# Performance work log

Hardware: AMD Instinct MI355X
Metric: run time of the kernel (lower is better)

The kernel has to match this reference:

```python
import jax, jax.numpy as jnp
import numpy as np

N, CIN, COUT = 8, 256, 512
HEADS, DK, DV = 8, 256, 256
MAP = 32          # H = W = map_size
KS, PAD = 3, 1
DKH = DK // HEADS  # 32
DVH = DV // HEADS  # 32
CONV_OUT = COUT - DV  # 256


def conv2d(x, w, b, stride=1, padding=0):
    out = jax.lax.conv_general_dilated(
        x, w, (stride, stride), [(padding, padding), (padding, padding)],
        dimension_numbers=("NCHW", "OIHW", "NCHW"))
    return out + b[None, :, None, None]


def rel_to_abs(x):
    # x: [B, G, L, 2L-1] relative logits -> [B, G, L, L] absolute (skewing trick)
    B, G, L, _ = x.shape
    x = jnp.pad(x, ((0, 0), (0, 0), (0, 0), (0, 1)))          # [B,G,L,2L]
    flat = x.reshape(B, G, L * 2 * L)
    flat = jnp.pad(flat, ((0, 0), (0, 0), (0, L - 1)))
    return flat.reshape(B, G, L + 1, 2 * L - 1)[:, :, :L, L - 1:]


def setup_inputs() -> dict:
    key = jax.random.key(0)
    ks = jax.random.split(key, 16)
    def w(k, shape, fan_in):
        return jax.random.normal(k, shape, jnp.float32) * (fan_in ** -0.5)
    inp = {
        "x": jax.random.normal(ks[0], (N, CIN, MAP, MAP), jnp.float32),
        "conv_w": w(ks[1], (CONV_OUT, CIN, KS, KS), CIN * KS * KS),
        "conv_b": jnp.zeros((CONV_OUT,), jnp.float32),
        "q_w": w(ks[2], (DK, CIN, KS, KS), CIN * KS * KS),
        "q_b": jnp.zeros((DK,), jnp.float32),
        "k_w": w(ks[3], (DK, CIN, KS, KS), CIN * KS * KS),
        "k_b": jnp.zeros((DK,), jnp.float32),
        "v_w": w(ks[4], (DV, CIN, KS, KS), CIN * KS * KS),
        "v_b": jnp.zeros((DV,), jnp.float32),
        "attn_w": w(ks[5], (DV, DV, 1, 1), DV),
        "attn_b": jnp.zeros((DV,), jnp.float32),
        "width_mat": jax.random.normal(ks[6], (2 * MAP - 1, DKH), jnp.float32) * (DKH ** -0.5),
        "height_mat": jax.random.normal(ks[7], (2 * MAP - 1, DKH), jnp.float32) * (DKH ** -0.5),
    }
    return inp


def reference(x, conv_w, conv_b, q_w, q_b, k_w, k_b, v_w, v_b,
              attn_w, attn_b, width_mat, height_mat):
    conv_maps = conv2d(x, conv_w, conv_b, 1, PAD)            # [N, 256, H, W]
    H = W = MAP
    q = conv2d(x, q_w, q_b, 1, PAD).reshape(N, HEADS, DKH, H, W)
    k = conv2d(x, k_w, k_b, 1, PAD).reshape(N, HEADS, DKH, H, W)
    v = conv2d(x, v_w, v_b, 1, PAD).reshape(N, HEADS, DVH, H, W)

    qf = q.reshape(N, HEADS, DKH, H * W)
    kf = k.reshape(N, HEADS, DKH, H * W)
    vf = v.reshape(N, HEADS, DVH, H * W)
    logits = jnp.einsum("nhdq,nhdk->nhqk", qf, kf)           # [N,h,HW,HW]

    qp = q.transpose(0, 1, 3, 4, 2)                          # [N,h,H,W,dkh]
    # width relative logits: depends on (hq, wq, wk), broadcast over hk
    rel_w = jnp.einsum("nhyxd,rd->nhyxr", qp, width_mat)     # [N,h,H,W,2W-1]
    abs_w = rel_to_abs(rel_w.reshape(N, HEADS * H, W, 2 * W - 1)
                       ).reshape(N, HEADS, H, W, W)          # [N,h,hq,wq,wk]
    # height relative logits: depends on (wq, hq, hk), broadcast over wk
    rel_h = jnp.einsum("nhyxd,rd->nhxyr", qp, height_mat)    # [N,h,W,H,2H-1]
    abs_h = rel_to_abs(rel_h.reshape(N, HEADS * W, H, 2 * H - 1)
                       ).reshape(N, HEADS, W, H, H)          # [N,h,wq,hq,hk]

    w_bias = abs_w[:, :, :, :, None, :]                      # [N,h,hq,wq,1,wk]
    h_bias = abs_h.transpose(0, 1, 3, 2, 4)[..., None]       # [N,h,hq,wq,hk,1]
    logits = (logits.reshape(N, HEADS, H, W, H, W) + h_bias + w_bias
              ).reshape(N, HEADS, H * W, H * W)
    logits = logits * (DKH ** -0.5)

    weights = jax.nn.softmax(logits, axis=-1)
    attn = jnp.einsum("nhqk,nhdk->nhqd", weights, vf)        # [N,h,HW,dvh]
    # faithful to torch .view quirk: row-major reshape [HW,dvh] -> [dvh,H,W]
    attn_maps = attn.reshape(N, HEADS * DVH, H, W)
    attn_maps = conv2d(attn_maps, attn_w, attn_b, 1, 0)
    return jnp.concatenate([conv_maps, attn_maps], axis=1)
```

## Files before the change

kernel.cpp:

```cpp
#include <hip/hip_runtime.h>
#include <hip/hip_bf16.h>


typedef __attribute__((ext_vector_type(8))) __bf16 bf16x8;
typedef __attribute__((ext_vector_type(4))) float f32x4;
typedef unsigned short u16;
typedef unsigned int u32;
typedef __attribute__((ext_vector_type(8))) u16 u16x8;

#define GLD(gp, lp) __builtin_amdgcn_global_load_lds( \
    (const __attribute__((address_space(1))) u32*)(gp), \
    (__attribute__((address_space(3))) u32*)(lp), 16, 0, 0)

static __device__ __forceinline__ u16 f2bf(float f) {
  u32 u = __builtin_bit_cast(u32, f);
  u += 0x7fffu + ((u >> 16) & 1u);
  return (u16)(u >> 16);
}
static __device__ __forceinline__ float bf2f(u16 h) {
  return __builtin_bit_cast(float, (u32)h << 16);
}

__global__ void k_cast_w(const float* __restrict__ conv_w, const float* __restrict__ q_w,
                         const float* __restrict__ k_w, const float* __restrict__ v_w,
                         const float* __restrict__ attn_w,
                         u16* __restrict__ W9, u16* __restrict__ W1) {
  int stride = gridDim.x * blockDim.x;
  for (int t = blockIdx.x * blockDim.x + threadIdx.x; t < 1024 * 2304; t += stride) {
    int row = t / 2304;
    int rem = t - row * 2304;
    int t9 = rem >> 8, c = rem & 255;
    const float* src = row < 256 ? conv_w : row < 512 ? q_w : row < 768 ? k_w : v_w;
    W9[t] = f2bf(src[(row & 255) * 2304 + c * 9 + t9]);
  }
  for (int t = blockIdx.x * blockDim.x + threadIdx.x; t < 256 * 256; t += stride)
    W1[t] = f2bf(attn_w[t]);
}

__global__ void k_xT(const float* __restrict__ x, u16* __restrict__ xT,
                     u16* __restrict__ zpage) {
  if (blockIdx.x == 0 && threadIdx.x < 512) zpage[threadIdx.x] = 0;
  __shared__ float t[32][33];
  int b = blockIdx.x;
  int sb = b & 31, cb = (b >> 5) & 7, n = b >> 8;
  int s0 = sb << 5, c0 = cb << 5;
  int ls = threadIdx.x & 31, lc = threadIdx.x >> 5;
#pragma unroll
  for (int i = 0; i < 4; ++i) {
    int c = lc + i * 8;
    t[c][ls] = x[(((n << 8) + c0 + c) << 10) + s0 + ls];
  }
  __syncthreads();
#pragma unroll
  for (int i = 0; i < 4; ++i) {
    int s = lc + i * 8;
    xT[(((n << 10) + s0 + s) << 8) + c0 + ls] = f2bf(t[ls][s]);
  }
}

__global__ __launch_bounds__(256) void k_gemm_conv(
    const u16* __restrict__ A, const u16* __restrict__ xT, const u16* __restrict__ zpage,
    float* __restrict__ out,
    u16* __restrict__ qb, u16* __restrict__ kb, u16* __restrict__ vb,
    const float* __restrict__ conv_b, const float* __restrict__ q_b,
    const float* __restrict__ k_b, const float* __restrict__ v_b) {
  __shared__ u16 As[8192], Bs[8192];
  f32x4 acc[4][4] = {};
  const int tid = threadIdx.x;
  const int wave = tid >> 6, lane = tid & 63;
  const int wr = wave >> 1, wc = wave & 1;
  const int lr = lane & 15, lk = lane >> 4;
  const int srow = lane >> 3;
  const int scol = (lane & 7) << 3;
  const int bm = blockIdx.x, bn = blockIdx.y;

  int bn_y[4], bn_x[4], bn_base[4];
#pragma unroll
  for (int i = 0; i < 4; ++i) {
    int seg = i * 4 + wave;
    int col = bn * 128 + seg * 8 + srow;
    int n = col >> 10, s = col & 1023;
    bn_y[i] = s >> 5;
    bn_x[i] = s & 31;
    bn_base[i] = n << 10;
  }

  for (int k0 = 0; k0 < 2304; k0 += 64) {
    int t9 = k0 >> 8;
    int dy = t9 / 3 - 1, dx = t9 - (t9 / 3) * 3 - 1;
    int c0 = k0 & 255;
#pragma unroll
    for (int i = 0; i < 4; ++i) {
      int seg = i * 4 + wave;
      GLD(A + (bm * 128 + seg * 8 + srow) * 2304 + k0 + scol, As + seg * 512);
      int sy = bn_y[i] + dy, sx = bn_x[i] + dx;
      bool ok = ((u32)sy < 32u) && ((u32)sx < 32u);
      const u16* src = ok ? (xT + (((bn_base[i] + (sy << 5) + sx)) << 8) + c0 + scol)
                          : (zpage + scol);
      GLD(src, Bs + seg * 512);
    }
    __syncthreads();
#pragma unroll
    for (int kk = 0; kk < 2; ++kk) {
      bf16x8 af[4], bv[4];
#pragma unroll
      for (int m = 0; m < 4; ++m)
        af[m] = *(const bf16x8*)&As[(wr * 64 + m * 16 + lr) * 64 + kk * 32 + lk * 8];
#pragma unroll
      for (int n = 0; n < 4; ++n)
        bv[n] = *(const bf16x8*)&Bs[(wc * 64 + n * 16 + lr) * 64 + kk * 32 + lk * 8];
#pragma unroll
      for (int m = 0; m < 4; ++m)
#pragma unroll
        for (int n = 0; n < 4; ++n)
          acc[m][n] = __builtin_amdgcn_mfma_f32_16x16x32_bf16(af[m], bv[n], acc[m][n], 0, 0, 0);
    }
    __syncthreads();
  }

  const int row0 = bm * 128 + wr * 64 + lk * 4;
  const int col0 = bn * 128 + wc * 64 + lr;
#pragma unroll
  for (int m = 0; m < 4; ++m) {
#pragma unroll
    for (int n = 0; n < 4; ++n) {
      int col = col0 + n * 16;
      int nn = col >> 10, s = col & 1023;
#pragma unroll
      for (int j = 0; j < 4; ++j) {
        int c = row0 + m * 16 + j;
        float v = acc[m][n][j];
        if (c < 256) {
          out[((nn << 9) + c) * 1024 + s] = v + conv_b[c];
        } else if (c < 512) {
          int cc = c - 256;
          qb[((((nn << 3) + (cc >> 5)) << 10) + s) * 32 + (cc & 31)] = f2bf(v + q_b[cc]);
        } else if (c < 768) {
          int cc = c - 512;
          kb[((((nn << 3) + (cc >> 5)) << 10) + s) * 32 + (cc & 31)] = f2bf(v + k_b[cc]);
        } else {
          int cc = c - 768;
          vb[((nn << 8) + cc) * 1024 + s] = f2bf(v + v_b[cc]);
        }
      }
    }
  }
}

__global__ __launch_bounds__(256) void k_bias(const u16* __restrict__ qb,
                                              const float* __restrict__ wm,
                                              const float* __restrict__ hm,
                                              float* __restrict__ Bw, float* __restrict__ Bh) {
  int pos = blockIdx.x * blockDim.x + threadIdx.x;
  int s = pos & 1023;
  int y = s >> 5, xx = s & 31;
  float q[32];
  const u16x8* q8 = (const u16x8*)(qb + pos * 32);
#pragma unroll
  for (int v = 0; v < 4; ++v) {
    u16x8 w = q8[v];
#pragma unroll
    for (int e = 0; e < 8; ++e) q[v * 8 + e] = bf2f(w[e]);
  }
  float* bwo = Bw + pos * 32;
  float* bho = Bh + pos * 32;
#pragma unroll 4
  for (int r = 0; r < 32; ++r) {
    const f32x4* wr = (const f32x4*)(wm + (r - xx + 31) * 32);
    const f32x4* hr = (const f32x4*)(hm + (r - y + 31) * 32);
    float aw = 0.f, ah = 0.f;
#pragma unroll
    for (int i = 0; i < 8; ++i) {
      f32x4 wv = wr[i], hv = hr[i];
#pragma unroll
      for (int e = 0; e < 4; ++e) {
        float qd = q[i * 4 + e];
        aw += qd * wv[e];
        ah += qd * hv[e];
      }
    }
    bwo[r] = aw;
    bho[r] = ah;
  }
}

__global__ __launch_bounds__(256) void k_attn(
    const u16* __restrict__ qb, const u16* __restrict__ kb, const u16* __restrict__ vb,
    const float* __restrict__ Bw, const float* __restrict__ Bh, u16* __restrict__ AMT) {
  __shared__ u16 Pl[4][1024];
  const int wave = threadIdx.x >> 6, lane = threadIdx.x & 63;
  const int task = blockIdx.x * 4 + wave;
  const int nh = task >> 6, qg = task & 63;
  const int n = nh >> 3, h = nh & 7;
  const int qbase = qg << 4;
  const int lr = lane & 15, lg = lane >> 4;

  bf16x8 aq = *(const bf16x8*)&qb[((nh << 10) + qbase + lr) * 32 + lg * 8];

  float Bwr[2][4];
#pragma unroll
  for (int p = 0; p < 2; ++p)
#pragma unroll
    for (int j = 0; j < 4; ++j)
      Bwr[p][j] = Bw[((nh << 10) + qbase + lg * 4 + j) * 32 + p * 16 + lr];

  float mrow[4] = {-1e30f, -1e30f, -1e30f, -1e30f};
  float lrow[4] = {0.f, 0.f, 0.f, 0.f};
  f32x4 o[2] = {};
  u16* pl = Pl[wave];

  for (int kt = 0; kt < 16; ++kt) {
    f32x4 zero = {0.f, 0.f, 0.f, 0.f};
    f32x4 sf_[4];
#pragma unroll
    for (int f = 0; f < 4; ++f) {
      bf16x8 bk = *(const bf16x8*)&kb[((nh << 10) + (kt << 6) + f * 16 + lr) * 32 + lg * 8];
      sf_[f] = __builtin_amdgcn_mfma_f32_16x16x32_bf16(aq, bk, zero, 0, 0, 0);
    }
    float Bhr[2][4];
#pragma unroll
    for (int p = 0; p < 2; ++p)
#pragma unroll
      for (int j = 0; j < 4; ++j)
        Bhr[p][j] = Bh[((nh << 10) + qbase + lg * 4 + j) * 32 + (kt << 1) + p];
    float tv[4][4];
#pragma unroll
    for (int f = 0; f < 4; ++f)
#pragma unroll
      for (int j = 0; j < 4; ++j)
        tv[f][j] = (sf_[f][j] + Bhr[f >> 1][j] + Bwr[f & 1][j]) * 0.17677669529663687f;

    float pv[4][4], sf[4];
#pragma unroll
    for (int j = 0; j < 4; ++j) {
      float vmax = fmaxf(fmaxf(tv[0][j], tv[1][j]), fmaxf(tv[2][j], tv[3][j]));
#pragma unroll
      for (int d = 1; d < 16; d <<= 1) vmax = fmaxf(vmax, __shfl_xor(vmax, d, 64));
      float mn = fmaxf(mrow[j], vmax);
      sf[j] = __expf(mrow[j] - mn);
      mrow[j] = mn;
      float sum = 0.f;
#pragma unroll
      for (int f = 0; f < 4; ++f) {
        float e = __expf(tv[f][j] - mn);
        pv[f][j] = e;
        sum += e;
      }
#pragma unroll
      for (int d = 1; d < 16; d <<= 1) sum += __shfl_xor(sum, d, 64);
      lrow[j] = lrow[j] * sf[j] + sum;
    }
#pragma unroll
    for (int dn = 0; dn < 2; ++dn)
#pragma unroll
      for (int j = 0; j < 4; ++j) o[dn][j] *= sf[j];

#pragma unroll
    for (int f = 0; f < 4; ++f)
#pragma unroll
      for (int j = 0; j < 4; ++j)
        pl[(lg * 4 + j) * 64 + f * 16 + lr] = f2bf(pv[f][j]);
    asm volatile("s_waitcnt lgkmcnt(0)" ::: "memory");
    bf16x8 pa0 = *(const bf16x8*)&pl[lr * 64 + lg * 8];
    bf16x8 pa1 = *(const bf16x8*)&pl[lr * 64 + 32 + lg * 8];
#pragma unroll
    for (int dn = 0; dn < 2; ++dn) {
      bf16x8 bv0 = *(const bf16x8*)&vb[((n << 8) + (h << 5) + dn * 16 + lr) * 1024 + (kt << 6) + lg * 8];
      o[dn] = __builtin_amdgcn_mfma_f32_16x16x32_bf16(pa0, bv0, o[dn], 0, 0, 0);
      bf16x8 bv1 = *(const bf16x8*)&vb[((n << 8) + (h << 5) + dn * 16 + lr) * 1024 + (kt << 6) + 32 + lg * 8];
      o[dn] = __builtin_amdgcn_mfma_f32_16x16x32_bf16(pa1, bv1, o[dn], 0, 0, 0);
    }
  }
#pragma unroll
  for (int dn = 0; dn < 2; ++dn)
#pragma unroll
    for (int j = 0; j < 4; ++j) {
      int q = qbase + lg * 4 + j;
      int d = dn * 16 + lr;
      float v = o[dn][j] / lrow[j];
      AMT[((n << 10) + ((q & 31) << 5) + d) * 256 + (h << 5) + (q >> 5)] = f2bf(v);
    }
}

static __device__ __forceinline__ void gemm_core(const u16* __restrict__ A,
                                                 const u16* __restrict__ B, int K,
                                                 u16* As, u16* Bs, f32x4 acc[4][4]) {
  const int tid = threadIdx.x;
  const int wave = tid >> 6, lane = tid & 63;
  const int wr = wave >> 1, wc = wave & 1;
  const int lr = lane & 15, lk = lane >> 4;
  const int srow = lane >> 3;
  const int scol = (lane & 7) << 3;
  const int bm = blockIdx.x, bn = blockIdx.y;
  for (int k0 = 0; k0 < K; k0 += 64) {
#pragma unroll
    for (int i = 0; i < 4; ++i) {
      int seg = i * 4 + wave;
      GLD(A + (bm * 128 + seg * 8 + srow) * K + k0 + scol, As + seg * 512);
      GLD(B + (bn * 128 + seg * 8 + srow) * K + k0 + scol, Bs + seg * 512);
    }
    __syncthreads();
#pragma unroll
    for (int kk = 0; kk < 2; ++kk) {
      bf16x8 af[4], bv[4];
#pragma unroll
      for (int m = 0; m < 4; ++m)
        af[m] = *(const bf16x8*)&As[(wr * 64 + m * 16 + lr) * 64 + kk * 32 + lk * 8];
#pragma unroll
      for (int n = 0; n < 4; ++n)
        bv[n] = *(const bf16x8*)&Bs[(wc * 64 + n * 16 + lr) * 64 + kk * 32 + lk * 8];
#pragma unroll
      for (int m = 0; m < 4; ++m)
#pragma unroll
        for (int n = 0; n < 4; ++n)
          acc[m][n] = __builtin_amdgcn_mfma_f32_16x16x32_bf16(af[m], bv[n], acc[m][n], 0, 0, 0);
    }
    __syncthreads();
  }
}

__global__ __launch_bounds__(256) void k_gemm_out(
    const u16* __restrict__ A, const u16* __restrict__ B, float* __restrict__ out,
    const float* __restrict__ attn_b) {
  __shared__ u16 As[8192], Bs[8192];
  f32x4 acc[4][4] = {};
  gemm_core(A, B, 256, As, Bs, acc);
  const int tid = threadIdx.x;
  const int wave = tid >> 6, lane = tid & 63;
  const int wr = wave >> 1, wc = wave & 1;
  const int lr = lane & 15, lk = lane >> 4;
  const int row0 = blockIdx.x * 128 + wr * 64 + lk * 4;
  const int col0 = blockIdx.y * 128 + wc * 64 + lr;
#pragma unroll
  for (int m = 0; m < 4; ++m) {
#pragma unroll
    for (int n = 0; n < 4; ++n) {
      int col = col0 + n * 16;
      int nn = col >> 10, s = col & 1023;
#pragma unroll
      for (int j = 0; j < 4; ++j) {
        int c = row0 + m * 16 + j;
        out[((nn << 9) + 256 + c) * 1024 + s] = acc[m][n][j] + attn_b[c];
      }
    }
  }
}

extern "C" void kernel_launch(void* const* d_in, const int* in_sizes, int n_in,
                              void* d_out, int out_size, void* d_ws, size_t ws_size,
                              hipStream_t stream) {
  const float* x      = (const float*)d_in[0];
  const float* conv_w = (const float*)d_in[1];
  const float* conv_b = (const float*)d_in[2];
  const float* q_w    = (const float*)d_in[3];
  const float* q_b    = (const float*)d_in[4];
  const float* k_w    = (const float*)d_in[5];
  const float* k_b    = (const float*)d_in[6];
  const float* v_w    = (const float*)d_in[7];
  const float* v_b    = (const float*)d_in[8];
  const float* attn_w = (const float*)d_in[9];
  const float* attn_b = (const float*)d_in[10];
  const float* wm     = (const float*)d_in[11];
  const float* hm     = (const float*)d_in[12];
  float* out = (float*)d_out;
  char* ws = (char*)d_ws;

  u16*   W9   = (u16*)(ws + 0);
  u16*   W1   = (u16*)(ws + 4718592);
  u16*   xT   = (u16*)(ws + 4849664);
  u16*   zpg  = (u16*)(ws + 9043968);
  u16*   qbf  = (u16*)(ws + 9044992);
  u16*   kbf  = (u16*)(ws + 13239296);
  u16*   vbf  = (u16*)(ws + 17433600);
  float* Bw   = (float*)(ws + 21627904);
  float* Bh   = (float*)(ws + 30016512);
  u16*   AMT  = (u16*)(ws + 38405120);

  hipLaunchKernelGGL(k_cast_w, dim3(2048), dim3(256), 0, stream,
                     conv_w, q_w, k_w, v_w, attn_w, W9, W1);
  hipLaunchKernelGGL(k_xT, dim3(2048), dim3(256), 0, stream, x, xT, zpg);
  hipLaunchKernelGGL(k_gemm_conv, dim3(8, 64), dim3(256), 0, stream,
                     W9, xT, zpg, out, qbf, kbf, vbf, conv_b, q_b, k_b, v_b);
  hipLaunchKernelGGL(k_bias, dim3(256), dim3(256), 0, stream, qbf, wm, hm, Bw, Bh);
  hipLaunchKernelGGL(k_attn, dim3(1024), dim3(256), 0, stream, qbf, kbf, vbf, Bw, Bh, AMT);
  hipLaunchKernelGGL(k_gemm_out, dim3(2, 64), dim3(256), 0, stream, W1, AMT, out, attn_b);
}
```

Measured before the change: 294.7 us.

## Double-buffer LDS in conv and output GEMMs, coalesce weight cast via shared memory

Both GEMM kernels now use two LDS buffers per operand and issue the async global-to-LDS loads for the next K tile before running the MFMAs on the current one. This hides load latency behind compute, at the cost of doubling LDS use per block, which may lower occupancy. The weight cast kernel now gives one block per row and stages the row in shared memory, so global reads are contiguous instead of strided. A sched_barrier is also added in the attention kernel to stop the compiler reordering across the LDS wait.

Result: no change. 297.5 us (+1.0%).

```diff
diff --git a/kernel.cpp b/kernel.cpp
--- a/kernel.cpp
+++ b/kernel.cpp
@@ -21,20 +21,24 @@
   return __builtin_bit_cast(float, (u32)h << 16);
 }
 
-__global__ void k_cast_w(const float* __restrict__ conv_w, const float* __restrict__ q_w,
-                         const float* __restrict__ k_w, const float* __restrict__ v_w,
-                         const float* __restrict__ attn_w,
-                         u16* __restrict__ W9, u16* __restrict__ W1) {
-  int stride = gridDim.x * blockDim.x;
-  for (int t = blockIdx.x * blockDim.x + threadIdx.x; t < 1024 * 2304; t += stride) {
-    int row = t / 2304;
-    int rem = t - row * 2304;
-    int t9 = rem >> 8, c = rem & 255;
-    const float* src = row < 256 ? conv_w : row < 512 ? q_w : row < 768 ? k_w : v_w;
-    W9[t] = f2bf(src[(row & 255) * 2304 + c * 9 + t9]);
-  }
-  for (int t = blockIdx.x * blockDim.x + threadIdx.x; t < 256 * 256; t += stride)
-    W1[t] = f2bf(attn_w[t]);
+__global__ __launch_bounds__(256) void k_cast_w(
+    const float* __restrict__ conv_w, const float* __restrict__ q_w,
+    const float* __restrict__ k_w, const float* __restrict__ v_w,
+    const float* __restrict__ attn_w, u16* __restrict__ W9, u16* __restrict__ W1) {
+  __shared__ float t[2304];
+  int row = blockIdx.x;
+  const float* src = row < 256 ? conv_w : row < 512 ? q_w : row < 768 ? k_w : v_w;
+  const float* sr = src + (row & 255) * 2304;
+#pragma unroll
+  for (int i = threadIdx.x; i < 2304; i += 256) t[i] = sr[i];
+  __syncthreads();
+  u16* dr = W9 + row * 2304;
+#pragma unroll
+  for (int i = threadIdx.x; i < 2304; i += 256) {
+    int t9 = i >> 8, c = i & 255;
+    dr[i] = f2bf(t[c * 9 + t9]);
+  }
+  if (row < 256) W1[row * 256 + threadIdx.x] = f2bf(attn_w[row * 256 + threadIdx.x]);
 }
 
 __global__ void k_xT(const float* __restrict__ x, u16* __restrict__ xT,
@@ -64,7 +68,7 @@
     u16* __restrict__ qb, u16* __restrict__ kb, u16* __restrict__ vb,
     const float* __restrict__ conv_b, const float* __restrict__ q_b,
     const float* __restrict__ k_b, const float* __restrict__ v_b) {
-  __shared__ u16 As[8192], Bs[8192];
+  __shared__ u16 As[2][8192], Bs[2][8192];
   f32x4 acc[4][4] = {};
   const int tid = threadIdx.x;
   const int wave = tid >> 6, lane = tid & 63;
@@ -85,30 +89,36 @@
     bn_base[i] = n << 10;
   }
 
-  for (int k0 = 0; k0 < 2304; k0 += 64) {
+  auto stage = [&](int buf, int k0) {
     int t9 = k0 >> 8;
     int dy = t9 / 3 - 1, dx = t9 - (t9 / 3) * 3 - 1;
     int c0 = k0 & 255;
 #pragma unroll
     for (int i = 0; i < 4; ++i) {
       int seg = i * 4 + wave;
-      GLD(A + (bm * 128 + seg * 8 + srow) * 2304 + k0 + scol, As + seg * 512);
+      GLD(A + (bm * 128 + seg * 8 + srow) * 2304 + k0 + scol, &As[buf][seg * 512]);
       int sy = bn_y[i] + dy, sx = bn_x[i] + dx;
       bool ok = ((u32)sy < 32u) && ((u32)sx < 32u);
-      const u16* src = ok ? (xT + (((bn_base[i] + (sy << 5) + sx)) << 8) + c0 + scol)
+      const u16* src = ok ? (xT + ((bn_base[i] + (sy << 5) + sx) << 8) + c0 + scol)
                           : (zpage + scol);
-      GLD(src, Bs + seg * 512);
-    }
-    __syncthreads();
+      GLD(src, &Bs[buf][seg * 512]);
+    }
+  };
+
+  stage(0, 0);
+  __syncthreads();
+  int cur = 0;
+  for (int kt = 0; kt < 36; ++kt) {
+    if (kt + 1 < 36) stage(cur ^ 1, (kt + 1) * 64);
 #pragma unroll
     for (int kk = 0; kk < 2; ++kk) {
       bf16x8 af[4], bv[4];
 #pragma unroll
       for (int m = 0; m < 4; ++m)
-        af[m] = *(const bf16x8*)&As[(wr * 64 + m * 16 + lr) * 64 + kk * 32 + lk * 8];
+        af[m] = *(const bf16x8*)&As[cur][(wr * 64 + m * 16 + lr) * 64 + kk * 32 + lk * 8];
 #pragma unroll
       for (int n = 0; n < 4; ++n)
-        bv[n] = *(const bf16x8*)&Bs[(wc * 64 + n * 16 + lr) * 64 + kk * 32 + lk * 8];
+        bv[n] = *(const bf16x8*)&Bs[cur][(wc * 64 + n * 16 + lr) * 64 + kk * 32 + lk * 8];
 #pragma unroll
       for (int m = 0; m < 4; ++m)
 #pragma unroll
@@ -116,6 +126,7 @@
           acc[m][n] = __builtin_amdgcn_mfma_f32_16x16x32_bf16(af[m], bv[n], acc[m][n], 0, 0, 0);
     }
     __syncthreads();
+    cur ^= 1;
   }
 
   const int row0 = bm * 128 + wr * 64 + lk * 4;
@@ -261,6 +272,7 @@
       for (int j = 0; j < 4; ++j)
         pl[(lg * 4 + j) * 64 + f * 16 + lr] = f2bf(pv[f][j]);
     asm volatile("s_waitcnt lgkmcnt(0)" ::: "memory");
+    __builtin_amdgcn_sched_barrier(0);
     bf16x8 pa0 = *(const bf16x8*)&pl[lr * 64 + lg * 8];
     bf16x8 pa1 = *(const bf16x8*)&pl[lr * 64 + 32 + lg * 8];
 #pragma unroll
@@ -284,7 +296,8 @@
 
 static __device__ __forceinline__ void gemm_core(const u16* __restrict__ A,
                                                  const u16* __restrict__ B, int K,
-                                                 u16* As, u16* Bs, f32x4 acc[4][4]) {
+                                                 u16 (*As)[8192], u16 (*Bs)[8192],
+                                                 f32x4 acc[4][4]) {
   const int tid = threadIdx.x;
   const int wave = tid >> 6, lane = tid & 63;
   const int wr = wave >> 1, wc = wave & 1;
@@ -292,23 +305,29 @@
   const int srow = lane >> 3;
   const int scol = (lane & 7) << 3;
   const int bm = blockIdx.x, bn = blockIdx.y;
-  for (int k0 = 0; k0 < K; k0 += 64) {
+  auto stage = [&](int buf, int k0) {
 #pragma unroll
     for (int i = 0; i < 4; ++i) {
       int seg = i * 4 + wave;
-      GLD(A + (bm * 128 + seg * 8 + srow) * K + k0 + scol, As + seg * 512);
-      GLD(B + (bn * 128 + seg * 8 + srow) * K + k0 + scol, Bs + seg * 512);
-    }
-    __syncthreads();
+      GLD(A + (bm * 128 + seg * 8 + srow) * K + k0 + scol, &As[buf][seg * 512]);
+      GLD(B + (bn * 128 + seg * 8 + srow) * K + k0 + scol, &Bs[buf][seg * 512]);
+    }
+  };
+  stage(0, 0);
+  __syncthreads();
+  int cur = 0;
+  const int nt = K >> 6;
+  for (int kt = 0; kt < nt; ++kt) {
+    if (kt + 1 < nt) stage(cur ^ 1, (kt + 1) << 6);
 #pragma unroll
     for (int kk = 0; kk < 2; ++kk) {
       bf16x8 af[4], bv[4];
 #pragma unroll
       for (int m = 0; m < 4; ++m)
-        af[m] = *(const bf16x8*)&As[(wr * 64 + m * 16 + lr) * 64 + kk * 32 + lk * 8];
+        af[m] = *(const bf16x8*)&As[cur][(wr * 64 + m * 16 + lr) * 64 + kk * 32 + lk * 8];
 #pragma unroll
       for (int n = 0; n < 4; ++n)
-        bv[n] = *(const bf16x8*)&Bs[(wc * 64 + n * 16 + lr) * 64 + kk * 32 + lk * 8];
+        bv[n] = *(const bf16x8*)&Bs[cur][(wc * 64 + n * 16 + lr) * 64 + kk * 32 + lk * 8];
 #pragma unroll
       for (int m = 0; m < 4; ++m)
 #pragma unroll
@@ -316,13 +335,14 @@
           acc[m][n] = __builtin_amdgcn_mfma_f32_16x16x32_bf16(af[m], bv[n], acc[m][n], 0, 0, 0);
     }
     __syncthreads();
+    cur ^= 1;
   }
 }
 
 __global__ __launch_bounds__(256) void k_gemm_out(
     const u16* __restrict__ A, const u16* __restrict__ B, float* __restrict__ out,
     const float* __restrict__ attn_b) {
-  __shared__ u16 As[8192], Bs[8192];
+  __shared__ u16 As[2][8192], Bs[2][8192];
   f32x4 acc[4][4] = {};
   gemm_core(A, B, 256, As, Bs, acc);
   const int tid = threadIdx.x;
@@ -376,7 +396,7 @@
   float* Bh   = (float*)(ws + 30016512);
   u16*   AMT  = (u16*)(ws + 38405120);
 
-  hipLaunchKernelGGL(k_cast_w, dim3(2048), dim3(256), 0, stream,
+  hipLaunchKernelGGL(k_cast_w, dim3(1024), dim3(256), 0, stream,
                      conv_w, q_w, k_w, v_w, attn_w, W9, W1);
   hipLaunchKernelGGL(k_xT, dim3(2048), dim3(256), 0, stream, x, xT, zpg);
   hipLaunchKernelGGL(k_gemm_conv, dim3(8, 64), dim3(256), 0, stream,
```
